# Optimization experiments

Hardware: AMD Instinct MI355X
Metric: run time of the kernel (lower is better)

Reference implementation:

```python
import jax, jax.numpy as jnp
import numpy as np

IOU_THRESHOLD = 0.5

def cxcywh_to_xyxy(b):
    cx, cy, w, h = jnp.split(b, 4, axis=-1)
    return jnp.concatenate([cx - 0.5 * w, cy - 0.5 * h, cx + 0.5 * w, cy + 0.5 * h], axis=-1)

def batched_giou(p_xyxy, t_xyxy):
    # p_xyxy: [B, N, 4], t_xyxy: [B, T, 4] -> giou: [B, N, T]
    p = p_xyxy[:, :, None, :]  # [B, N, 1, 4]
    t = t_xyxy[:, None, :, :]  # [B, 1, T, 4]
    area_p = (p_xyxy[..., 2] - p_xyxy[..., 0]) * (p_xyxy[..., 3] - p_xyxy[..., 1])  # [B, N]
    area_t = (t_xyxy[..., 2] - t_xyxy[..., 0]) * (t_xyxy[..., 3] - t_xyxy[..., 1])  # [B, T]
    lt = jnp.maximum(p[..., :2], t[..., :2])
    rb = jnp.minimum(p[..., 2:], t[..., 2:])
    wh = jnp.clip(rb - lt, 0.0)
    inter = wh[..., 0] * wh[..., 1]  # [B, N, T]
    union = area_p[:, :, None] + area_t[:, None, :] - inter
    iou = inter / union
    # enclosing box
    lt_e = jnp.minimum(p[..., :2], t[..., :2])
    rb_e = jnp.maximum(p[..., 2:], t[..., 2:])
    wh_e = jnp.clip(rb_e - lt_e, 0.0)
    area_e = wh_e[..., 0] * wh_e[..., 1]
    return iou - (area_e - union) / area_e

def setup_inputs() -> dict:
    key = jax.random.key(0)
    k1, k2 = jax.random.split(key)
    B, N, T = 128, 900, 300
    pred_boxes = jax.random.uniform(k1, (B, N, 4), dtype=jnp.float32)
    target_boxes = jax.random.uniform(k2, (B, T, 4), dtype=jnp.float32)
    target_mask = jnp.ones((B, T), dtype=bool)
    return {"pred_boxes": pred_boxes, "target_boxes": target_boxes, "target_mask": target_mask}

def reference(pred_boxes, target_boxes, target_mask):
    # pred_boxes: [B, N, 4] cxcywh; target_boxes: [B, T, 4] cxcywh (padded)
    p_xyxy = cxcywh_to_xyxy(pred_boxes)
    t_xyxy = cxcywh_to_xyxy(target_boxes)
    giou = batched_giou(p_xyxy, t_xyxy)  # [B, N, T]
    max_iou = jnp.max(giou, axis=1)      # [B, T] best GIoU per target
    pred_idx = jnp.argmax(giou, axis=1)  # [B, T] matched query per target
    valid = target_mask & (max_iou >= IOU_THRESHOLD)  # [B, T] match kept
    return pred_idx, valid, max_iou
```

## Files before the change

kernel.cpp:

```cpp
#include <hip/hip_runtime.h>


#define BB 128
#define NN 900
#define TT 300
#define TCHUNK 64
#define TBLOCKS 5
#define NSPLIT 5
#define NPB 180
#define NPW 45
#define MARGIN 2e-5f

__device__ __forceinline__ float giou_exact(float4 pb, float4 tb) {
#pragma clang fp contract(off)
    float px0 = pb.x - 0.5f * pb.z, py0 = pb.y - 0.5f * pb.w;
    float px1 = pb.x + 0.5f * pb.z, py1 = pb.y + 0.5f * pb.w;
    float tx0 = tb.x - 0.5f * tb.z, ty0 = tb.y - 0.5f * tb.w;
    float tx1 = tb.x + 0.5f * tb.z, ty1 = tb.y + 0.5f * tb.w;
    float pa = (px1 - px0) * (py1 - py0);
    float ta = (tx1 - tx0) * (ty1 - ty0);
    float w  = fmaxf(fminf(px1, tx1) - fmaxf(px0, tx0), 0.f);
    float h  = fmaxf(fminf(py1, ty1) - fmaxf(py0, ty0), 0.f);
    float inter = w * h;
    float uni   = pa + ta - inter;
    float iou   = inter / uni;
    float ew = fmaxf(fmaxf(px1, tx1) - fminf(px0, tx0), 0.f);
    float eh = fmaxf(fmaxf(py1, ty1) - fminf(py0, ty0), 0.f);
    float ea = ew * eh;
    return iou - (ea - uni) / ea;
}

__global__ __launch_bounds__(256) void matcher_prep_kernel(
    const float4* __restrict__ pred,
    float4* __restrict__ pxy)
{
    const int i = blockIdx.x * 256 + threadIdx.x;
    if (i >= BB * NN) return;
    const float4 pb = pred[i];
    float4 q;
    q.x = pb.x - 0.5f * pb.z;
    q.y = pb.y - 0.5f * pb.w;
    q.z = pb.x + 0.5f * pb.z;
    q.w = pb.y + 0.5f * pb.w;
    const float pw = q.z - q.x;
    const float ph = q.w - q.y;
    float4 c;
    c.x = pw * ph;
    c.y = pw;
    c.z = ph;
    c.w = 0.f;
    pxy[2 * i]     = q;
    pxy[2 * i + 1] = c;
}

__global__ __launch_bounds__(256, 8) void matcher_scan_kernel(
    const float4* __restrict__ pxy,
    const float* __restrict__ tgt,
    float* __restrict__ pbest,
    float* __restrict__ psec,
    int*   __restrict__ pidx)
{
    __shared__ float rbv[256], rsv[256];
    __shared__ int   riv[256];

    const int ns  = blockIdx.x % NSPLIT;
    const int tc  = (blockIdx.x / NSPLIT) % TBLOCKS;
    const int b   = blockIdx.x / (NSPLIT * TBLOCKS);
    const int tid = threadIdx.x;
    const int tl  = tid & 63;
    const int ng  = tid >> 6;
    const int t   = tc * TCHUNK + tl;

    float tx0 = 0.f, ty0 = 0.f, tx1 = 0.f, ty1 = 0.f;
    float ta = 0.f, tw = 0.f, th = 0.f;
    if (t < TT) {
        const float4 tb = ((const float4*)tgt)[b * TT + t];
        tx0 = tb.x - 0.5f * tb.z;
        ty0 = tb.y - 0.5f * tb.w;
        tx1 = tb.x + 0.5f * tb.z;
        ty1 = tb.y + 0.5f * tb.w;
        tw = tx1 - tx0;
        th = ty1 - ty0;
        ta = tw * th;
    }

    const int k0 = ng * NPW;
    const int kbase =
        __builtin_amdgcn_readfirstlane(2 * (b * NN + ns * NPB + k0));
    const float4* pp = pxy + kbase;

    float best = -INFINITY, second = -INFINITY;
    int   bidxl = 0;
    #pragma unroll 9
    for (int k = 0; k < NPW; ++k) {
        const float4 q = pp[2 * k];
        const float4 c = pp[2 * k + 1];

        const float m1x = fminf(q.z, tx1);
        const float M0x = fmaxf(q.x, tx0);
        const float wr  = m1x - M0x;
        const float w   = fmaxf(wr, 0.f);
        const float m1y = fminf(q.w, ty1);
        const float M0y = fmaxf(q.y, ty0);
        const float hr  = m1y - M0y;
        const float h   = fmaxf(hr, 0.f);
        const float inter = w * h;
        const float uni   = (c.x + ta) - inter;

        const float ew = (c.y + tw) - wr;
        const float eh = (c.z + th) - hr;
        const float ea = ew * eh;

        const float num = fmaf(inter, ea, uni * (uni - ea));
        const float g   = num * __builtin_amdgcn_rcpf(uni * ea);

        second = __builtin_amdgcn_fmed3f(g, best, second);
        if (g > best) bidxl = k;
        best = fmaxf(best, g);
    }
    int bidx = k0 + bidxl;

    rbv[tid] = best; rsv[tid] = second; riv[tid] = bidx;
    __syncthreads();

    if (ng == 0 && t < TT) {
        for (int s = 1; s < 4; ++s) {
            const float ob = rbv[s * 64 + tl];
            const float os = rsv[s * 64 + tl];
            const int   oi = riv[s * 64 + tl];
            second = fmaxf(fminf(best, ob), fmaxf(second, os));
            if (ob > best) { best = ob; bidx = oi; }
        }
        const int bt = b * TT + t;
        pbest[ns * BB * TT + bt] = best;
        psec [ns * BB * TT + bt] = second;
        pidx [ns * BB * TT + bt] = ns * NPB + bidx;
    }
}

__global__ __launch_bounds__(256) void matcher_finish_kernel(
    const float* __restrict__ pbest,
    const float* __restrict__ psec,
    const int*   __restrict__ pidx,
    const float* __restrict__ pred,
    const float* __restrict__ tgt,
    const unsigned char* __restrict__ mask,
    float* __restrict__ out)
{
    __shared__ int sflag[256];
    __shared__ int scount;

    const int tid = threadIdx.x;
    const int bt  = blockIdx.x * 256 + tid;
    if (tid == 0) scount = 0;
    __syncthreads();

    float best = -INFINITY, second = -INFINITY;
    int   bidx = 0;
    #pragma unroll
    for (int s = 0; s < NSPLIT; ++s) {
        const float ob = pbest[s * BB * TT + bt];
        const float os = psec [s * BB * TT + bt];
        const int   oi = pidx [s * BB * TT + bt];
        second = fmaxf(fminf(best, ob), fmaxf(second, os));
        if (ob > best) { best = ob; bidx = oi; }
    }

    if (best - second > MARGIN) {
        const int b = bt / TT;
        const float4 pb = ((const float4*)pred)[b * NN + bidx];
        const float4 tb = ((const float4*)tgt)[bt];
        const float g = giou_exact(pb, tb);
        const bool valid = (mask[bt] != 0) && (g >= 0.5f);
        out[bt]               = (float)bidx;
        out[BB * TT + bt]     = valid ? 1.f : 0.f;
        out[2 * BB * TT + bt] = g;
    } else {
        const int pos = atomicAdd(&scount, 1);
        sflag[pos] = tid;
    }
    __syncthreads();

    const int cnt  = scount;
    const int lane = tid & 63;
    const int ng   = tid >> 6;
    for (int f = ng; f < cnt; f += 4) {
        const int fbt = blockIdx.x * 256 + sflag[f];
        const int b   = fbt / TT;
        const float4 tb = ((const float4*)tgt)[fbt];

        float bestx = -INFINITY;
        int   bix   = NN;
        for (int n = lane; n < NN; n += 64) {
            const float4 pb = ((const float4*)pred)[b * NN + n];
            const float g = giou_exact(pb, tb);
            if (g > bestx) { bestx = g; bix = n; }
        }
        for (int off = 32; off >= 1; off >>= 1) {
            const float ob = __shfl_xor(bestx, off);
            const int   oi = __shfl_xor(bix, off);
            if (ob > bestx || (ob == bestx && oi < bix)) { bestx = ob; bix = oi; }
        }
        if (lane == 0) {
            const bool valid = (mask[fbt] != 0) && (bestx >= 0.5f);
            out[fbt]               = (float)bix;
            out[BB * TT + fbt]     = valid ? 1.f : 0.f;
            out[2 * BB * TT + fbt] = bestx;
        }
    }
}

extern "C" void kernel_launch(void* const* d_in, const int* in_sizes, int n_in,
                              void* d_out, int out_size, void* d_ws, size_t ws_size,
                              hipStream_t stream) {
    const float* pred = (const float*)d_in[0];
    const float* tgt  = (const float*)d_in[1];
    const unsigned char* mask = (const unsigned char*)d_in[2];
    float* out = (float*)d_out;

    const size_t seg = (size_t)NSPLIT * BB * TT * 4;
    char* ws = (char*)d_ws;
    float*  pbest = (float*)ws;
    float*  psec  = (float*)(ws + seg);
    int*    pidx  = (int*)  (ws + 2 * seg);
    float4* pxy   = (float4*)(ws + 3 * seg);

    matcher_prep_kernel<<<dim3((BB * NN + 255) / 256), dim3(256), 0, stream>>>(
        (const float4*)pred, pxy);
    matcher_scan_kernel<<<dim3(BB * TBLOCKS * NSPLIT), dim3(256), 0, stream>>>(
        pxy, tgt, pbest, psec, pidx);
    matcher_finish_kernel<<<dim3(BB * TT / 256), dim3(256), 0, stream>>>(
        pbest, psec, pidx, pred, tgt, mask, out);
}
```

Measured before the change: 100.1 us.

## Fuse pred-box prep into scan kernel and process two targets per thread

Removes the separate prep kernel. Each scan block now converts its slice of predicted boxes to corner form and stages them in shared memory. Each thread in the first two target chunks evaluates two targets per loaded pred box, which cuts the block count from 5 to 3 target chunks per batch and reuses shared-memory loads. The price is a redundant prep per target chunk, an extra barrier, a tail chunk that uses only a quarter of its work, and higher register pressure under launch bound 8.

```diff
diff --git a/kernel.cpp b/kernel.cpp
--- a/kernel.cpp
+++ b/kernel.cpp
@@ -4,8 +4,6 @@
 #define BB 128
 #define NN 900
 #define TT 300
-#define TCHUNK 64
-#define TBLOCKS 5
 #define NSPLIT 5
 #define NPB 180
 #define NPW 45
@@ -30,111 +28,161 @@
     return iou - (ea - uni) / ea;
 }
 
-__global__ __launch_bounds__(256) void matcher_prep_kernel(
+__device__ __forceinline__ void giou_step(
+    const float4 q, const float4 c,
+    const float tx0, const float ty0, const float tx1, const float ty1,
+    const float tw, const float th, const float ta, const int k,
+    float& best, float& second, int& bidxl)
+{
+    const float m1x = fminf(q.z, tx1);
+    const float M0x = fmaxf(q.x, tx0);
+    const float wr  = m1x - M0x;
+    const float w   = fmaxf(wr, 0.f);
+    const float m1y = fminf(q.w, ty1);
+    const float M0y = fmaxf(q.y, ty0);
+    const float hr  = m1y - M0y;
+    const float h   = fmaxf(hr, 0.f);
+    const float inter = w * h;
+    const float uni   = (c.x + ta) - inter;
+    const float ew = (c.y + tw) - wr;
+    const float eh = (c.z + th) - hr;
+    const float ea = ew * eh;
+    const float num = fmaf(inter, ea, uni * (uni - ea));
+    const float g   = num * __builtin_amdgcn_rcpf(uni * ea);
+    second = __builtin_amdgcn_fmed3f(g, best, second);
+    if (g > best) bidxl = k;
+    best = fmaxf(best, g);
+}
+
+__device__ __forceinline__ void load_target(
+    const float4* __restrict__ tgt, const int idx,
+    float& tx0, float& ty0, float& tx1, float& ty1,
+    float& tw, float& th, float& ta)
+{
+    const float4 tb = tgt[idx];
+    tx0 = tb.x - 0.5f * tb.z;
+    ty0 = tb.y - 0.5f * tb.w;
+    tx1 = tb.x + 0.5f * tb.z;
+    ty1 = tb.y + 0.5f * tb.w;
+    tw = tx1 - tx0;
+    th = ty1 - ty0;
+    ta = tw * th;
+}
+
+__global__ __launch_bounds__(256, 8) void matcher_scan_kernel(
     const float4* __restrict__ pred,
-    float4* __restrict__ pxy)
-{
-    const int i = blockIdx.x * 256 + threadIdx.x;
-    if (i >= BB * NN) return;
-    const float4 pb = pred[i];
-    float4 q;
-    q.x = pb.x - 0.5f * pb.z;
-    q.y = pb.y - 0.5f * pb.w;
-    q.z = pb.x + 0.5f * pb.z;
-    q.w = pb.y + 0.5f * pb.w;
-    const float pw = q.z - q.x;
-    const float ph = q.w - q.y;
-    float4 c;
-    c.x = pw * ph;
-    c.y = pw;
-    c.z = ph;
-    c.w = 0.f;
-    pxy[2 * i]     = q;
-    pxy[2 * i + 1] = c;
-}
-
-__global__ __launch_bounds__(256, 8) void matcher_scan_kernel(
-    const float4* __restrict__ pxy,
-    const float* __restrict__ tgt,
+    const float4* __restrict__ tgt,
     float* __restrict__ pbest,
     float* __restrict__ psec,
     int*   __restrict__ pidx)
 {
-    __shared__ float rbv[256], rsv[256];
-    __shared__ int   riv[256];
+    __shared__ float4 sq[NPB];
+    __shared__ float4 scc[NPB];
+    __shared__ float rb1[256], rs1[256], rb2[256], rs2[256];
+    __shared__ int   ri1[256], ri2[256];
 
     const int ns  = blockIdx.x % NSPLIT;
-    const int tc  = (blockIdx.x / NSPLIT) % TBLOCKS;
-    const int b   = blockIdx.x / (NSPLIT * TBLOCKS);
+    const int tc  = (blockIdx.x / NSPLIT) % 3;
+    const int b   = blockIdx.x / (NSPLIT * 3);
     const int tid = threadIdx.x;
     const int tl  = tid & 63;
     const int ng  = tid >> 6;
-    const int t   = tc * TCHUNK + tl;
-
-    float tx0 = 0.f, ty0 = 0.f, tx1 = 0.f, ty1 = 0.f;
-    float ta = 0.f, tw = 0.f, th = 0.f;
-    if (t < TT) {
-        const float4 tb = ((const float4*)tgt)[b * TT + t];
-        tx0 = tb.x - 0.5f * tb.z;
-        ty0 = tb.y - 0.5f * tb.w;
-        tx1 = tb.x + 0.5f * tb.z;
-        ty1 = tb.y + 0.5f * tb.w;
-        tw = tx1 - tx0;
-        th = ty1 - ty0;
-        ta = tw * th;
-    }
+
+    if (tid < NPB) {
+        const float4 pb = pred[b * NN + ns * NPB + tid];
+        float4 q;
+        q.x = pb.x - 0.5f * pb.z;
+        q.y = pb.y - 0.5f * pb.w;
+        q.z = pb.x + 0.5f * pb.z;
+        q.w = pb.y + 0.5f * pb.w;
+        const float pw = q.z - q.x;
+        const float ph = q.w - q.y;
+        sq[tid]  = q;
+        scc[tid] = make_float4(pw * ph, pw, ph, 0.f);
+    }
+    __syncthreads();
 
     const int k0 = ng * NPW;
-    const int kbase =
-        __builtin_amdgcn_readfirstlane(2 * (b * NN + ns * NPB + k0));
-    const float4* pp = pxy + kbase;
-
-    float best = -INFINITY, second = -INFINITY;
-    int   bidxl = 0;
-    #pragma unroll 9
-    for (int k = 0; k < NPW; ++k) {
-        const float4 q = pp[2 * k];
-        const float4 c = pp[2 * k + 1];
-
-        const float m1x = fminf(q.z, tx1);
-        const float M0x = fmaxf(q.x, tx0);
-        const float wr  = m1x - M0x;
-        const float w   = fmaxf(wr, 0.f);
-        const float m1y = fminf(q.w, ty1);
-        const float M0y = fmaxf(q.y, ty0);
-        const float hr  = m1y - M0y;
-        const float h   = fmaxf(hr, 0.f);
-        const float inter = w * h;
-        const float uni   = (c.x + ta) - inter;
-
-        const float ew = (c.y + tw) - wr;
-        const float eh = (c.z + th) - hr;
-        const float ea = ew * eh;
-
-        const float num = fmaf(inter, ea, uni * (uni - ea));
-        const float g   = num * __builtin_amdgcn_rcpf(uni * ea);
-
-        second = __builtin_amdgcn_fmed3f(g, best, second);
-        if (g > best) bidxl = k;
-        best = fmaxf(best, g);
-    }
-    int bidx = k0 + bidxl;
-
-    rbv[tid] = best; rsv[tid] = second; riv[tid] = bidx;
-    __syncthreads();
-
-    if (ng == 0 && t < TT) {
-        for (int s = 1; s < 4; ++s) {
-            const float ob = rbv[s * 64 + tl];
-            const float os = rsv[s * 64 + tl];
-            const int   oi = riv[s * 64 + tl];
-            second = fmaxf(fminf(best, ob), fmaxf(second, os));
-            if (ob > best) { best = ob; bidx = oi; }
-        }
-        const int bt = b * TT + t;
-        pbest[ns * BB * TT + bt] = best;
-        psec [ns * BB * TT + bt] = second;
-        pidx [ns * BB * TT + bt] = ns * NPB + bidx;
+
+    if (tc < 2) {
+        const int t1 = tc * 128 + tl;
+        const int t2 = t1 + 64;
+        float ax0, ay0, ax1, ay1, aw, ah, aa;
+        float bx0, by0, bx1, by1, bw, bh, ba;
+        load_target(tgt, b * TT + t1, ax0, ay0, ax1, ay1, aw, ah, aa);
+        load_target(tgt, b * TT + t2, bx0, by0, bx1, by1, bw, bh, ba);
+
+        float best1 = -INFINITY, sec1 = -INFINITY;
+        float best2 = -INFINITY, sec2 = -INFINITY;
+        int   i1 = 0, i2 = 0;
+        #pragma unroll 9
+        for (int k = 0; k < NPW; ++k) {
+            const float4 q = sq[k0 + k];
+            const float4 c = scc[k0 + k];
+            giou_step(q, c, ax0, ay0, ax1, ay1, aw, ah, aa, k, best1, sec1, i1);
+            giou_step(q, c, bx0, by0, bx1, by1, bw, bh, ba, k, best2, sec2, i2);
+        }
+        int bi1 = k0 + i1, bi2 = k0 + i2;
+
+        rb1[tid] = best1; rs1[tid] = sec1; ri1[tid] = bi1;
+        rb2[tid] = best2; rs2[tid] = sec2; ri2[tid] = bi2;
+        __syncthreads();
+
+        if (ng == 0) {
+            for (int s = 1; s < 4; ++s) {
+                const float ob1 = rb1[s * 64 + tl];
+                const float os1 = rs1[s * 64 + tl];
+                const int   oi1 = ri1[s * 64 + tl];
+                sec1 = fmaxf(fminf(best1, ob1), fmaxf(sec1, os1));
+                if (ob1 > best1) { best1 = ob1; bi1 = oi1; }
+                const float ob2 = rb2[s * 64 + tl];
+                const float os2 = rs2[s * 64 + tl];
+                const int   oi2 = ri2[s * 64 + tl];
+                sec2 = fmaxf(fminf(best2, ob2), fmaxf(sec2, os2));
+                if (ob2 > best2) { best2 = ob2; bi2 = oi2; }
+            }
+            const int bt1 = b * TT + t1;
+            const int bt2 = b * TT + t2;
+            pbest[ns * BB * TT + bt1] = best1;
+            psec [ns * BB * TT + bt1] = sec1;
+            pidx [ns * BB * TT + bt1] = ns * NPB + bi1;
+            pbest[ns * BB * TT + bt2] = best2;
+            psec [ns * BB * TT + bt2] = sec2;
+            pidx [ns * BB * TT + bt2] = ns * NPB + bi2;
+        }
+    } else {
+        const int t = 256 + tl;
+        float ax0 = 0.f, ay0 = 0.f, ax1 = 0.f, ay1 = 0.f;
+        float aw = 0.f, ah = 0.f, aa = 0.f;
+        if (t < TT)
+            load_target(tgt, b * TT + t, ax0, ay0, ax1, ay1, aw, ah, aa);
+
+        float best = -INFINITY, second = -INFINITY;
+        int   bidxl = 0;
+        #pragma unroll 9
+        for (int k = 0; k < NPW; ++k) {
+            const float4 q = sq[k0 + k];
+            const float4 c = scc[k0 + k];
+            giou_step(q, c, ax0, ay0, ax1, ay1, aw, ah, aa, k, best, second, bidxl);
+        }
+        int bidx = k0 + bidxl;
+
+        rb1[tid] = best; rs1[tid] = second; ri1[tid] = bidx;
+        __syncthreads();
+
+        if (ng == 0 && t < TT) {
+            for (int s = 1; s < 4; ++s) {
+                const float ob = rb1[s * 64 + tl];
+                const float os = rs1[s * 64 + tl];
+                const int   oi = ri1[s * 64 + tl];
+                second = fmaxf(fminf(best, ob), fmaxf(second, os));
+                if (ob > best) { best = ob; bidx = oi; }
+            }
+            const int bt = b * TT + t;
+            pbest[ns * BB * TT + bt] = best;
+            psec [ns * BB * TT + bt] = second;
+            pidx [ns * BB * TT + bt] = ns * NPB + bidx;
+        }
     }
 }
 
@@ -220,15 +268,12 @@
 
     const size_t seg = (size_t)NSPLIT * BB * TT * 4;
     char* ws = (char*)d_ws;
-    float*  pbest = (float*)ws;
-    float*  psec  = (float*)(ws + seg);
-    int*    pidx  = (int*)  (ws + 2 * seg);
-    float4* pxy   = (float4*)(ws + 3 * seg);
-
-    matcher_prep_kernel<<<dim3((BB * NN + 255) / 256), dim3(256), 0, stream>>>(
-        (const float4*)pred, pxy);
-    matcher_scan_kernel<<<dim3(BB * TBLOCKS * NSPLIT), dim3(256), 0, stream>>>(
-        pxy, tgt, pbest, psec, pidx);
+    float* pbest = (float*)ws;
+    float* psec  = (float*)(ws + seg);
+    int*   pidx  = (int*)  (ws + 2 * seg);
+
+    matcher_scan_kernel<<<dim3(BB * 3 * NSPLIT), dim3(256), 0, stream>>>(
+        (const float4*)pred, (const float4*)tgt, pbest, psec, pidx);
     matcher_finish_kernel<<<dim3(BB * TT / 256), dim3(256), 0, stream>>>(
         pbest, psec, pidx, pred, tgt, mask, out);
 }
```

New measurement: 96.06 us. -4.1%, faster.

## Fuse prep, scan and finish into one kernel with LDS-staged predictions

Applied to the files above, without the earlier changes.

Replaces the three-kernel pipeline (prep, split scan, finish) with a single kernel per (batch, target-chunk) block. Each block converts all 900 predictions to xyxy once into shared memory, and each of its four waves scans 225 of them. The block then merges the per-wave results and handles the ambiguous near-tie targets in place. This removes two launches, the global workspace round-trips and the partial-result merge. In exchange the grid shrinks to 640 blocks and each prediction is converted five times (once per target chunk), with pred area and width recomputed inside the loop, which lowers parallelism.

```diff
diff --git a/kernel.cpp b/kernel.cpp
--- a/kernel.cpp
+++ b/kernel.cpp
@@ -4,11 +4,9 @@
 #define BB 128
 #define NN 900
 #define TT 300
-#define TCHUNK 64
-#define TBLOCKS 5
-#define NSPLIT 5
-#define NPB 180
-#define NPW 45
+#define TCHUNKS 5
+#define WPB 4
+#define PSPLIT 225
 #define MARGIN 2e-5f
 
 __device__ __forceinline__ float giou_exact(float4 pb, float4 tb) {
@@ -30,71 +28,57 @@
     return iou - (ea - uni) / ea;
 }
 
-__global__ __launch_bounds__(256) void matcher_prep_kernel(
+__global__ __launch_bounds__(256, 4) void matcher_kernel(
     const float4* __restrict__ pred,
-    float4* __restrict__ pxy)
+    const float4* __restrict__ tgt,
+    const unsigned char* __restrict__ mask,
+    float* __restrict__ out)
 {
-    const int i = blockIdx.x * 256 + threadIdx.x;
-    if (i >= BB * NN) return;
-    const float4 pb = pred[i];
-    float4 q;
-    q.x = pb.x - 0.5f * pb.z;
-    q.y = pb.y - 0.5f * pb.w;
-    q.z = pb.x + 0.5f * pb.z;
-    q.w = pb.y + 0.5f * pb.w;
-    const float pw = q.z - q.x;
-    const float ph = q.w - q.y;
-    float4 c;
-    c.x = pw * ph;
-    c.y = pw;
-    c.z = ph;
-    c.w = 0.f;
-    pxy[2 * i]     = q;
-    pxy[2 * i + 1] = c;
-}
-
-__global__ __launch_bounds__(256, 8) void matcher_scan_kernel(
-    const float4* __restrict__ pxy,
-    const float* __restrict__ tgt,
-    float* __restrict__ pbest,
-    float* __restrict__ psec,
-    int*   __restrict__ pidx)
-{
+    __shared__ float4 sq[NN];
     __shared__ float rbv[256], rsv[256];
     __shared__ int   riv[256];
+    __shared__ int   sflag[64];
+    __shared__ int   scount;
 
-    const int ns  = blockIdx.x % NSPLIT;
-    const int tc  = (blockIdx.x / NSPLIT) % TBLOCKS;
-    const int b   = blockIdx.x / (NSPLIT * TBLOCKS);
+    const int tc  = blockIdx.x % TCHUNKS;
+    const int b   = blockIdx.x / TCHUNKS;
     const int tid = threadIdx.x;
     const int tl  = tid & 63;
     const int ng  = tid >> 6;
-    const int t   = tc * TCHUNK + tl;
 
-    float tx0 = 0.f, ty0 = 0.f, tx1 = 0.f, ty1 = 0.f;
-    float ta = 0.f, tw = 0.f, th = 0.f;
-    if (t < TT) {
-        const float4 tb = ((const float4*)tgt)[b * TT + t];
-        tx0 = tb.x - 0.5f * tb.z;
-        ty0 = tb.y - 0.5f * tb.w;
-        tx1 = tb.x + 0.5f * tb.z;
-        ty1 = tb.y + 0.5f * tb.w;
-        tw = tx1 - tx0;
-        th = ty1 - ty0;
-        ta = tw * th;
+    if (tid == 0) scount = 0;
+
+    for (int i = tid; i < NN; i += 256) {
+        const float4 pb = pred[b * NN + i];
+        float4 q;
+        q.x = pb.x - 0.5f * pb.z;
+        q.y = pb.y - 0.5f * pb.w;
+        q.z = pb.x + 0.5f * pb.z;
+        q.w = pb.y + 0.5f * pb.w;
+        sq[i] = q;
     }
+    __syncthreads();
 
-    const int k0 = ng * NPW;
-    const int kbase =
-        __builtin_amdgcn_readfirstlane(2 * (b * NN + ns * NPB + k0));
-    const float4* pp = pxy + kbase;
+    const int  t      = tc * 64 + tl;
+    const bool tvalid = (t < TT);
+    const float4 tb = tgt[b * TT + (tvalid ? t : 0)];
+    const float tx0 = tb.x - 0.5f * tb.z;
+    const float ty0 = tb.y - 0.5f * tb.w;
+    const float tx1 = tb.x + 0.5f * tb.z;
+    const float ty1 = tb.y + 0.5f * tb.w;
+    const float tw  = tx1 - tx0;
+    const float th  = ty1 - ty0;
+    const float ta  = tw * th;
 
+    const int k0 = ng * PSPLIT;
     float best = -INFINITY, second = -INFINITY;
     int   bidxl = 0;
     #pragma unroll 9
-    for (int k = 0; k < NPW; ++k) {
-        const float4 q = pp[2 * k];
-        const float4 c = pp[2 * k + 1];
+    for (int k = 0; k < PSPLIT; ++k) {
+        const float4 q = sq[k0 + k];
+        const float pw = q.z - q.x;
+        const float ph = q.w - q.y;
+        const float pa = pw * ph;
 
         const float m1x = fminf(q.z, tx1);
         const float M0x = fmaxf(q.x, tx0);
@@ -105,12 +89,10 @@
         const float hr  = m1y - M0y;
         const float h   = fmaxf(hr, 0.f);
         const float inter = w * h;
-        const float uni   = (c.x + ta) - inter;
-
-        const float ew = (c.y + tw) - wr;
-        const float eh = (c.z + th) - hr;
+        const float uni   = (pa + ta) - inter;
+        const float ew = (pw + tw) - wr;
+        const float eh = (ph + th) - hr;
         const float ea = ew * eh;
-
         const float num = fmaf(inter, ea, uni * (uni - ea));
         const float g   = num * __builtin_amdgcn_rcpf(uni * ea);
 
@@ -123,77 +105,43 @@
     rbv[tid] = best; rsv[tid] = second; riv[tid] = bidx;
     __syncthreads();
 
-    if (ng == 0 && t < TT) {
-        for (int s = 1; s < 4; ++s) {
+    if (ng == 0) {
+        for (int s = 1; s < WPB; ++s) {
             const float ob = rbv[s * 64 + tl];
             const float os = rsv[s * 64 + tl];
             const int   oi = riv[s * 64 + tl];
             second = fmaxf(fminf(best, ob), fmaxf(second, os));
             if (ob > best) { best = ob; bidx = oi; }
         }
-        const int bt = b * TT + t;
-        pbest[ns * BB * TT + bt] = best;
-        psec [ns * BB * TT + bt] = second;
-        pidx [ns * BB * TT + bt] = ns * NPB + bidx;
-    }
-}
 
-__global__ __launch_bounds__(256) void matcher_finish_kernel(
-    const float* __restrict__ pbest,
-    const float* __restrict__ psec,
-    const int*   __restrict__ pidx,
-    const float* __restrict__ pred,
-    const float* __restrict__ tgt,
-    const unsigned char* __restrict__ mask,
-    float* __restrict__ out)
-{
-    __shared__ int sflag[256];
-    __shared__ int scount;
-
-    const int tid = threadIdx.x;
-    const int bt  = blockIdx.x * 256 + tid;
-    if (tid == 0) scount = 0;
-    __syncthreads();
-
-    float best = -INFINITY, second = -INFINITY;
-    int   bidx = 0;
-    #pragma unroll
-    for (int s = 0; s < NSPLIT; ++s) {
-        const float ob = pbest[s * BB * TT + bt];
-        const float os = psec [s * BB * TT + bt];
-        const int   oi = pidx [s * BB * TT + bt];
-        second = fmaxf(fminf(best, ob), fmaxf(second, os));
-        if (ob > best) { best = ob; bidx = oi; }
-    }
-
-    if (best - second > MARGIN) {
-        const int b = bt / TT;
-        const float4 pb = ((const float4*)pred)[b * NN + bidx];
-        const float4 tb = ((const float4*)tgt)[bt];
-        const float g = giou_exact(pb, tb);
-        const bool valid = (mask[bt] != 0) && (g >= 0.5f);
-        out[bt]               = (float)bidx;
-        out[BB * TT + bt]     = valid ? 1.f : 0.f;
-        out[2 * BB * TT + bt] = g;
-    } else {
-        const int pos = atomicAdd(&scount, 1);
-        sflag[pos] = tid;
+        if (tvalid) {
+            const int bt = b * TT + t;
+            if (best - second > MARGIN) {
+                const float4 pb = pred[b * NN + bidx];
+                const float4 tbr = tgt[bt];
+                const float g = giou_exact(pb, tbr);
+                const bool valid = (mask[bt] != 0) && (g >= 0.5f);
+                out[bt]               = (float)bidx;
+                out[BB * TT + bt]     = valid ? 1.f : 0.f;
+                out[2 * BB * TT + bt] = g;
+            } else {
+                const int pos = atomicAdd(&scount, 1);
+                sflag[pos] = tl;
+            }
+        }
     }
     __syncthreads();
 
-    const int cnt  = scount;
-    const int lane = tid & 63;
-    const int ng   = tid >> 6;
-    for (int f = ng; f < cnt; f += 4) {
-        const int fbt = blockIdx.x * 256 + sflag[f];
-        const int b   = fbt / TT;
-        const float4 tb = ((const float4*)tgt)[fbt];
+    const int cnt = scount;
+    for (int f = ng; f < cnt; f += WPB) {
+        const int fbt = b * TT + tc * 64 + sflag[f];
+        const float4 tbr = tgt[fbt];
 
         float bestx = -INFINITY;
         int   bix   = NN;
-        for (int n = lane; n < NN; n += 64) {
-            const float4 pb = ((const float4*)pred)[b * NN + n];
-            const float g = giou_exact(pb, tb);
+        for (int n = tl; n < NN; n += 64) {
+            const float4 pb = pred[b * NN + n];
+            const float g = giou_exact(pb, tbr);
             if (g > bestx) { bestx = g; bix = n; }
         }
         for (int off = 32; off >= 1; off >>= 1) {
@@ -201,7 +149,7 @@
             const int   oi = __shfl_xor(bix, off);
             if (ob > bestx || (ob == bestx && oi < bix)) { bestx = ob; bix = oi; }
         }
-        if (lane == 0) {
+        if (tl == 0) {
             const bool valid = (mask[fbt] != 0) && (bestx >= 0.5f);
             out[fbt]               = (float)bix;
             out[BB * TT + fbt]     = valid ? 1.f : 0.f;
@@ -218,17 +166,6 @@
     const unsigned char* mask = (const unsigned char*)d_in[2];
     float* out = (float*)d_out;
 
-    const size_t seg = (size_t)NSPLIT * BB * TT * 4;
-    char* ws = (char*)d_ws;
-    float*  pbest = (float*)ws;
-    float*  psec  = (float*)(ws + seg);
-    int*    pidx  = (int*)  (ws + 2 * seg);
-    float4* pxy   = (float4*)(ws + 3 * seg);
-
-    matcher_prep_kernel<<<dim3((BB * NN + 255) / 256), dim3(256), 0, stream>>>(
-        (const float4*)pred, pxy);
-    matcher_scan_kernel<<<dim3(BB * TBLOCKS * NSPLIT), dim3(256), 0, stream>>>(
-        pxy, tgt, pbest, psec, pidx);
-    matcher_finish_kernel<<<dim3(BB * TT / 256), dim3(256), 0, stream>>>(
-        pbest, psec, pidx, pred, tgt, mask, out);
+    matcher_kernel<<<dim3(BB * TCHUNKS), dim3(256), 0, stream>>>(
+        (const float4*)pred, (const float4*)tgt, mask, out);
 }
```

Result: no change. 99.95 us (-0.2%).
